# Optimization experiments

Measured on AMD Instinct MI355X. Metric: run time of the kernel, lower is better.

Reference implementation:

```python
import jax, jax.numpy as jnp
import numpy as np

N = 100_000   # nodes
E = 200_000   # directed edges
G = 2_500     # graphs in batch
F_NODE = 16
F_EDGE = 8
H1 = 32
H2 = 16


def setup_inputs() -> dict:
    key = jax.random.key(0)
    ks = jax.random.split(key, 24)
    p = lambda k, shape: 0.1 * jax.random.normal(k, shape, dtype=jnp.float32)
    inp = {
        "x": jax.random.normal(ks[0], (N, F_NODE), dtype=jnp.float32),
        "edge_attr": jax.random.normal(ks[1], (E, F_EDGE), dtype=jnp.float32),
        # edge-MLP for conv1: F_EDGE -> 16 -> F_NODE*H1
        "w_e1a": p(ks[2], (F_EDGE, 16)), "b_e1a": p(ks[3], (16,)),
        "w_e1b": p(ks[4], (16, F_NODE * H1)), "b_e1b": p(ks[5], (F_NODE * H1,)),
        "w_root1": p(ks[6], (F_NODE, H1)), "b_root1": p(ks[7], (H1,)),
        # edge-MLP for conv2: F_EDGE -> 16 -> H1*H2
        "w_e2a": p(ks[8], (F_EDGE, 16)), "b_e2a": p(ks[9], (16,)),
        "w_e2b": p(ks[10], (16, H1 * H2)), "b_e2b": p(ks[11], (H1 * H2,)),
        "w_root2": p(ks[12], (H1, H2)), "b_root2": p(ks[13], (H2,)),
        # attention-pool gate nn: F_NODE -> F_NODE -> 1
        "w_g1": p(ks[14], (F_NODE, F_NODE)), "b_g1": p(ks[15], (F_NODE,)),
        "w_g2": p(ks[16], (F_NODE, 1)), "b_g2": p(ks[17], (1,)),
        # head: (H2 + F_NODE) -> 8 -> 1
        "w_l1": p(ks[18], (H2 + F_NODE, 8)), "b_l1": p(ks[19], (8,)),
        "w_l2": p(ks[20], (8, 1)), "b_l2": p(ks[21], (1,)),
        "edge_index": jax.random.randint(ks[22], (2, E), 0, N),
        "batch": jnp.sort(jax.random.randint(ks[23], (N,), 0, G)),
    }
    return inp


def _nnconv(x, src, tgt, edge_attr, wa, ba, wb, bb, wr, br, in_c, out_c, n):
    # PyG NNConv: x_i' = x_i @ W_root + b + sum_{j->i} x_j @ Theta(e_ji)
    h = jax.nn.relu(edge_attr @ wa + ba)              # [E, 16]
    theta = (h @ wb + bb).reshape(-1, in_c, out_c)    # [E, in, out]
    msg = jnp.einsum('ei,eio->eo', x[src], theta)     # [E, out]
    agg = jax.ops.segment_sum(msg, tgt, num_segments=n)
    return x @ wr + br + agg


def reference(x, edge_attr, w_e1a, b_e1a, w_e1b, b_e1b, w_root1, b_root1,
              w_e2a, b_e2a, w_e2b, b_e2b, w_root2, b_root2,
              w_g1, b_g1, w_g2, b_g2, w_l1, b_l1, w_l2, b_l2,
              edge_index, batch):
    src, tgt = edge_index[0], edge_index[1]
    n = x.shape[0]

    # GlobalAttention pooling on raw node features (per-graph segment softmax)
    gate = jax.nn.relu(x @ w_g1 + b_g1) @ w_g2 + b_g2          # [N, 1]
    m = jax.ops.segment_max(gate, batch, num_segments=G)       # [G, 1]
    a = jnp.exp(gate - m[batch])
    s = jax.ops.segment_sum(a, batch, num_segments=G)
    x_att = jax.ops.segment_sum((a / s[batch]) * x, batch, num_segments=G)  # [G, F_NODE]

    # Two NNConv layers with ReLU
    h = jax.nn.relu(_nnconv(x, src, tgt, edge_attr, w_e1a, b_e1a, w_e1b, b_e1b,
                            w_root1, b_root1, F_NODE, H1, n))
    h = jax.nn.relu(_nnconv(h, src, tgt, edge_attr, w_e2a, b_e2a, w_e2b, b_e2b,
                            w_root2, b_root2, H1, H2, n))

    # global_mean_pool
    cnt = jax.ops.segment_sum(jnp.ones((n, 1), h.dtype), batch, num_segments=G)
    mean = jax.ops.segment_sum(h, batch, num_segments=G) / jnp.maximum(cnt, 1.0)

    z = jnp.concatenate([mean, x_att], axis=1)  # [G, H2 + F_NODE]
    # eval mode: dropout p=0.5 is identity; two linear layers, no activation between
    z = z @ w_l1 + b_l1
    z = z @ w_l2 + b_l2
    return z
```

## Files before the change

### kernel.cpp

```cpp
#include <hip/hip_runtime.h>
#include <hip/hip_bf16.h>

#define NN 100000
#define NE 200000
#define NG 2500
#define FN 16
#define FE 8
#define H1C 32
#define H2C 16
#define KH 16

typedef __attribute__((ext_vector_type(8))) short short8;
typedef __attribute__((ext_vector_type(4))) float f32x4;

__device__ __forceinline__ float bf2f(unsigned int u){
  union { unsigned int i; float f; } v; v.i = (u & 0xffffu) << 16; return v.f;
}
__device__ __forceinline__ unsigned short f2bf(float f){
  union { float f; unsigned int i; } u; u.f = f;
  unsigned int r = u.i + 0x7fffu + ((u.i >> 16) & 1u);
  return (unsigned short)(r >> 16);
}
__device__ __forceinline__ unsigned int pk2(float a, float b){
  return (unsigned int)f2bf(a) | ((unsigned int)f2bf(b) << 16);
}
__device__ __forceinline__ float rdf(const void* p, long i, bool isbf){
  return isbf ? bf2f(((const unsigned short*)p)[i]) : ((const float*)p)[i];
}
__device__ __forceinline__ int lower_bound_i(const int* __restrict__ a, int n, int v){
  int lo = 0, hi = n;
  while(lo < hi){ int mid = (lo + hi) >> 1; if(a[mid] < v) lo = mid + 1; else hi = mid; }
  return lo;
}
__device__ __forceinline__ bool detect_isbf(const void* __restrict__ x){
  const unsigned short* u = (const unsigned short*)x;
  int lane = threadIdx.x & 63;
  float f = bf2f(u[2*lane]);
  float a = fabsf(f);
  bool sane = (f == 0.0f) || (a > 1e-4f && a < 1e4f);
  unsigned long long b = __ballot(sane);
  return __popcll(b) >= 32;
}

#define NW 20
struct WArgs { const void* p[NW]; };
enum {
  OW_E1A=0,     OB_E1A=128,   OW_E1B=144,   OB_E1B=8336,  OW_R1=8848,  OB_R1=9360,
  OW_E2A=9392,  OB_E2A=9520,  OW_E2B=9536,  OB_E2B=17728, OW_R2=18240, OB_R2=18752,
  OW_G1=18768,  OB_G1=19024,  OW_G2=19040,  OB_G2=19056,
  OW_L1=19057,  OB_L1=19313,  OW_L2=19321,  OB_L2=19329
};

#define MB_A 76
#define MB_B (MB_A + 19)
#define MB_C (MB_B + 18)
#define MB_D (MB_C + 391)
#define MB_E (MB_D + 782)
__global__ void __launch_bounds__(256) mega1_kernel(
    const void* __restrict__ xin, const void* __restrict__ efin, WArgs w,
    const int* __restrict__ ei,
    float* __restrict__ wts, unsigned int* __restrict__ wpack1, unsigned int* __restrict__ wpack2,
    float* __restrict__ gate, float* __restrict__ xf, int* __restrict__ deg)
{
  int b = blockIdx.x, tid = threadIdx.x;
  if(b < MB_A){
    bool isbf = detect_isbf(xin);
    int i = b*256 + tid;
    if(i >= 19330) return;
    const int sz[NW] = {128,16,8192,512,512,32, 128,16,8192,512,512,16, 256,16,16,1, 256,8,8,1};
    int seg = 0; long base = 0;
    while(i - base >= sz[seg]){ base += sz[seg]; seg++; }
    wts[i] = rdf(w.p[seg], i - base, isbf);
    return;
  }
  if(b < MB_B){
    bool isbf = detect_isbf(xin);
    int j = (b - MB_A)*256 + tid;
    if(j >= 4736) return;
    int n = j / 148; int k = (j % 148) * 2;
    float v0 = 0.f, v1 = 0.f;
    if(k < 256)        v0 = rdf(w.p[2], (long)k*32 + n, isbf);
    else if(k < 272)   v0 = rdf(w.p[3], (long)(k-256)*32 + n, isbf);
    if(k+1 < 256)      v1 = rdf(w.p[2], (long)(k+1)*32 + n, isbf);
    else if(k+1 < 272) v1 = rdf(w.p[3], (long)(k+1-256)*32 + n, isbf);
    wpack1[j] = pk2(v0, v1);
    return;
  }
  if(b < MB_C){
    bool isbf = detect_isbf(xin);
    int j = (b - MB_B)*256 + tid;
    if(j >= 4416) return;
    int n = j / 276; int k = (j % 276) * 2;
    float v0 = 0.f, v1 = 0.f;
    if(k < 512)        v0 = rdf(w.p[8], (long)k*16 + n, isbf);
    else if(k < 544)   v0 = rdf(w.p[9], (long)(k-512)*16 + n, isbf);
    if(k+1 < 512)      v1 = rdf(w.p[8], (long)(k+1)*16 + n, isbf);
    else if(k+1 < 544) v1 = rdf(w.p[9], (long)(k+1-512)*16 + n, isbf);
    wpack2[j] = pk2(v0, v1);
    return;
  }
  if(b < MB_D){
    __shared__ float s_w1[FN*FN], s_b1[FN], s_w2[FN], s_b2v[1];
    bool isbf = detect_isbf(xin);
    if(tid < FN*FN) s_w1[tid] = rdf(w.p[12], tid, isbf);
    if(tid < FN){ s_b1[tid] = rdf(w.p[13], tid, isbf); s_w2[tid] = rdf(w.p[14], tid, isbf); }
    if(tid == 0) s_b2v[0] = rdf(w.p[15], 0, isbf);
    __syncthreads();
    int n = (b - MB_C)*256 + tid;
    if(n >= NN) return;
    float xv[FN];
    if(isbf){
      uint4 u0 = ((const uint4*)xin)[2*n], u1 = ((const uint4*)xin)[2*n+1];
      xv[0]=bf2f(u0.x); xv[1]=bf2f(u0.x>>16); xv[2]=bf2f(u0.y); xv[3]=bf2f(u0.y>>16);
      xv[4]=bf2f(u0.z); xv[5]=bf2f(u0.z>>16); xv[6]=bf2f(u0.w); xv[7]=bf2f(u0.w>>16);
      xv[8]=bf2f(u1.x); xv[9]=bf2f(u1.x>>16); xv[10]=bf2f(u1.y); xv[11]=bf2f(u1.y>>16);
      xv[12]=bf2f(u1.z); xv[13]=bf2f(u1.z>>16); xv[14]=bf2f(u1.w); xv[15]=bf2f(u1.w>>16);
    } else {
      #pragma unroll
      for(int q = 0; q < 4; q++){
        float4 v = ((const float4*)xin)[4*n + q];
        xv[q*4+0]=v.x; xv[q*4+1]=v.y; xv[q*4+2]=v.z; xv[q*4+3]=v.w;
      }
    }
    float4* xo = (float4*)(xf + (size_t)n*FN);
    #pragma unroll
    for(int q = 0; q < 4; q++) xo[q] = make_float4(xv[q*4+0], xv[q*4+1], xv[q*4+2], xv[q*4+3]);
    float g = s_b2v[0];
    #pragma unroll
    for(int j = 0; j < FN; j++){
      float hj = s_b1[j];
      #pragma unroll
      for(int i = 0; i < FN; i++) hj += xv[i] * s_w1[i*FN + j];
      hj = hj > 0.f ? hj : 0.f;
      g += hj * s_w2[j];
    }
    gate[n] = g;
    return;
  }
  {
    int e = (b - MB_D)*256 + tid;
    if(e < NE) atomicAdd(&deg[ei[NE + e]], 1);
  }
}

#define SCAN_NB 98
__global__ void __launch_bounds__(256) scan_kernel(
    const int* __restrict__ deg, int* __restrict__ rowptr, int* __restrict__ cursor,
    unsigned int* __restrict__ pub)
{
  __shared__ int s_thr[256];
  __shared__ int s_agg[SCAN_NB];
  __shared__ int s_bcast;
  int tid = threadIdx.x, bid = blockIdx.x;
  int base = bid*1024 + tid*4;
  int v0=0, v1=0, v2=0, v3=0;
  if(base + 3 < NN){
    int4 t4 = *(const int4*)(deg + base);
    v0=t4.x; v1=t4.y; v2=t4.z; v3=t4.w;
  } else {
    if(base+0 < NN) v0 = deg[base+0];
    if(base+1 < NN) v1 = deg[base+1];
    if(base+2 < NN) v2 = deg[base+2];
  }
  int e1 = v0, e2 = v0+v1, e3 = v0+v1+v2, tot = v0+v1+v2+v3;
  s_thr[tid] = tot;
  __syncthreads();
  for(int off = 1; off < 256; off <<= 1){
    int t = (tid >= off) ? s_thr[tid-off] : 0;
    __syncthreads();
    s_thr[tid] += t;
    __syncthreads();
  }
  int thr_excl = s_thr[tid] - tot;
  int agg = s_thr[255];
  if(tid == 0) atomicExch(&pub[bid], ((unsigned int)agg << 1) | 1u);
  if(tid < SCAN_NB){
    unsigned int v;
    do { v = atomicAdd(&pub[tid], 0u); } while((v & 1u) == 0u);
    s_agg[tid] = (int)(v >> 1);
  }
  __syncthreads();
  if(tid == 0){
    int acc = 0;
    for(int p = 0; p < bid; p++) acc += s_agg[p];
    s_bcast = acc;
  }
  __syncthreads();
  int ex = s_bcast + thr_excl;
  if(base + 3 < NN){
    int4 r = make_int4(ex, ex+e1, ex+e2, ex+e3);
    *(int4*)(rowptr + base) = r;
    *(int4*)(cursor + base) = r;
  } else {
    if(base+0 < NN){ rowptr[base+0]=ex;    cursor[base+0]=ex;    }
    if(base+1 < NN){ rowptr[base+1]=ex+e1; cursor[base+1]=ex+e1; }
    if(base+2 < NN){ rowptr[base+2]=ex+e2; cursor[base+2]=ex+e2; }
  }
  if(bid == 0 && tid == 0) rowptr[NN] = NE;
}

__global__ void __launch_bounds__(256) fill_edge_kernel(
    const int* __restrict__ ei, int* __restrict__ cursor,
    const void* __restrict__ efin, const float* __restrict__ wts, const void* __restrict__ xin,
    int* __restrict__ srcp, unsigned int* __restrict__ hpk1, unsigned int* __restrict__ hpk2)
{
  __shared__ float s_w1[FE*KH], s_b1[KH], s_w2[FE*KH], s_b2[KH];
  int tid = threadIdx.x;
  if(tid < FE*KH){ s_w1[tid] = wts[OW_E1A + tid]; s_w2[tid] = wts[OW_E2A + tid]; }
  if(tid < KH){ s_b1[tid] = wts[OB_E1A + tid]; s_b2[tid] = wts[OB_E2A + tid]; }
  bool isbf = detect_isbf(xin);
  __syncthreads();
  int e = blockIdx.x*256 + tid;
  if(e >= NE) return;
  int pos = atomicAdd(&cursor[ei[NE + e]], 1);
  srcp[pos] = ei[e];
  float ev[FE];
  if(isbf){
    uint4 u = ((const uint4*)efin)[e];
    ev[0]=bf2f(u.x); ev[1]=bf2f(u.x>>16); ev[2]=bf2f(u.y); ev[3]=bf2f(u.y>>16);
    ev[4]=bf2f(u.z); ev[5]=bf2f(u.z>>16); ev[6]=bf2f(u.w); ev[7]=bf2f(u.w>>16);
  } else {
    float4 a = ((const float4*)efin)[2*e], b = ((const float4*)efin)[2*e+1];
    ev[0]=a.x; ev[1]=a.y; ev[2]=a.z; ev[3]=a.w; ev[4]=b.x; ev[5]=b.y; ev[6]=b.z; ev[7]=b.w;
  }
  unsigned int o[8];
  #pragma unroll
  for(int d = 0; d < 8; d++){
    float h0 = s_b1[2*d], h1 = s_b1[2*d+1];
    #pragma unroll
    for(int k = 0; k < FE; k++){
      h0 += ev[k] * s_w1[k*KH + 2*d];
      h1 += ev[k] * s_w1[k*KH + 2*d+1];
    }
    h0 = h0 > 0.f ? h0 : 0.f; h1 = h1 > 0.f ? h1 : 0.f;
    o[d] = pk2(h0, h1);
  }
  uint4* p1 = (uint4*)(hpk1 + (size_t)pos*8);
  p1[0] = make_uint4(o[0],o[1],o[2],o[3]); p1[1] = make_uint4(o[4],o[5],o[6],o[7]);
  #pragma unroll
  for(int d = 0; d < 8; d++){
    float h0 = s_b2[2*d], h1 = s_b2[2*d+1];
    #pragma unroll
    for(int k = 0; k < FE; k++){
      h0 += ev[k] * s_w2[k*KH + 2*d];
      h1 += ev[k] * s_w2[k*KH + 2*d+1];
    }
    h0 = h0 > 0.f ? h0 : 0.f; h1 = h1 > 0.f ? h1 : 0.f;
    o[d] = pk2(h0, h1);
  }
  uint4* p2 = (uint4*)(hpk2 + (size_t)pos*8);
  p2[0] = make_uint4(o[0],o[1],o[2],o[3]); p2[1] = make_uint4(o[4],o[5],o[6],o[7]);
}

template<int IN, int OUT, bool ABF>
__global__ void __launch_bounds__(256) conv_mfma_kernel(
    const void* __restrict__ nodef, const unsigned int* __restrict__ hpk,
    const int* __restrict__ srcp, const unsigned short* __restrict__ wpack,
    unsigned short* __restrict__ msg)
{
  constexpr int KMF  = ((KH*IN + IN + 31)/32)*32;
  constexpr int KP   = KMF + 8;
  constexpr int NT   = OUT/16;
  constexpr int KS   = KMF/32;
  int tid = threadIdx.x;
  int lane = tid & 63, m = lane & 15, quad = lane >> 4;
  int wid = tid >> 6;
  int ebase = blockIdx.x*64 + wid*16;
  int em = ebase + m;
  int sn = srcp[em];
  int q1 = quad >> 1;
  int xoff = (IN == 16) ? ((quad & 1)*8) : (quad*8);
  float x8[8];
  short8 xb;
  if(ABF){
    uint4 u = *(const uint4*)((const unsigned short*)nodef + (size_t)sn*IN + xoff);
    unsigned int uu[4] = {u.x, u.y, u.z, u.w};
    #pragma unroll
    for(int k = 0; k < 4; k++){ x8[2*k] = bf2f(uu[k]); x8[2*k+1] = bf2f(uu[k] >> 16); }
    xb = *(short8*)&u;
  } else {
    const float4* xp = (const float4*)((const float*)nodef + (size_t)sn*IN + xoff);
    float4 v0 = xp[0], v1 = xp[1];
    x8[0]=v0.x; x8[1]=v0.y; x8[2]=v0.z; x8[3]=v0.w;
    x8[4]=v1.x; x8[5]=v1.y; x8[6]=v1.z; x8[7]=v1.w;
    unsigned int* xbp = (unsigned int*)&xb;
    #pragma unroll
    for(int k = 0; k < 4; k++) xbp[k] = pk2(x8[2*k], x8[2*k+1]);
  }
  unsigned int hu[8];
  {
    const uint4* hp = (const uint4*)(hpk + (size_t)em*8);
    uint4 u0 = hp[0], u1 = hp[1];
    hu[0]=u0.x; hu[1]=u0.y; hu[2]=u0.z; hu[3]=u0.w;
    hu[4]=u1.x; hu[5]=u1.y; hu[6]=u1.z; hu[7]=u1.w;
  }

  f32x4 acc[NT];
  #pragma unroll
  for(int nt = 0; nt < NT; nt++) acc[nt] = (f32x4){0.f,0.f,0.f,0.f};

  #pragma unroll
  for(int ks = 0; ks < KS; ks++){
    short8 a;
    if(ks < KS-1){
      float hv = (IN == 16) ? bf2f(hu[ks] >> (16*q1))
                            : bf2f(hu[ks >> 1] >> (16*(ks & 1)));
      unsigned int* ap = (unsigned int*)&a;
      #pragma unroll
      for(int k = 0; k < 4; k++) ap[k] = pk2(hv*x8[2*k], hv*x8[2*k+1]);
    } else {
      if(IN == 16) a = (quad < 2) ? xb : (short8){0,0,0,0,0,0,0,0};
      else         a = xb;
    }
    #pragma unroll
    for(int nt = 0; nt < NT; nt++){
      short8 b = *(const short8*)(wpack + (size_t)(nt*16 + m)*KP + ks*32 + quad*8);
      acc[nt] = __builtin_amdgcn_mfma_f32_16x16x32_bf16(a, b, acc[nt], 0, 0, 0);
    }
  }
  #pragma unroll
  for(int nt = 0; nt < NT; nt++)
    #pragma unroll
    for(int r = 0; r < 4; r++)
      msg[(size_t)(ebase + quad*4 + r)*OUT + nt*16 + m] = f2bf(acc[nt][r]);
}

__global__ void __launch_bounds__(256) gather1_kernel(
    const float* __restrict__ xf, const unsigned short* __restrict__ msg,
    const int* __restrict__ rowptr,
    const float* __restrict__ wr, const float* __restrict__ br,
    unsigned short* __restrict__ h1b)
{
  __shared__ float s_w[FN*H1C], s_b[H1C];
  for(int i = threadIdx.x; i < FN*H1C; i += 256) s_w[i] = wr[i];
  if(threadIdx.x < H1C) s_b[threadIdx.x] = br[threadIdx.x];
  __syncthreads();
  int g = blockIdx.x*256 + threadIdx.x;
  int n = g >> 3, q = g & 7;
  if(n >= NN) return;
  float a0 = s_b[q*4+0], a1 = s_b[q*4+1], a2 = s_b[q*4+2], a3 = s_b[q*4+3];
  int jb = rowptr[n], je = rowptr[n+1];
  for(int j = jb; j < je; j++){
    const unsigned int* mp = (const unsigned int*)(msg + (size_t)j*H1C + q*4);
    unsigned int u0 = mp[0], u1 = mp[1];
    a0 += bf2f(u0); a1 += bf2f(u0 >> 16); a2 += bf2f(u1); a3 += bf2f(u1 >> 16);
  }
  const float* xr = xf + (size_t)n*FN;
  #pragma unroll
  for(int i = 0; i < FN; i++){
    float xi = xr[i];
    a0 += xi*s_w[i*H1C + q*4+0]; a1 += xi*s_w[i*H1C + q*4+1];
    a2 += xi*s_w[i*H1C + q*4+2]; a3 += xi*s_w[i*H1C + q*4+3];
  }
  a0 = a0>0.f?a0:0.f; a1 = a1>0.f?a1:0.f; a2 = a2>0.f?a2:0.f; a3 = a3>0.f?a3:0.f;
  uint2 hb; hb.x = pk2(a0, a1); hb.y = pk2(a2, a3);
  *(uint2*)(h1b + (size_t)n*H1C + q*4) = hb;
}

__global__ void __launch_bounds__(256) gather2_kernel(
    const unsigned short* __restrict__ h1b, const unsigned short* __restrict__ msg,
    const int* __restrict__ rowptr,
    const float* __restrict__ wr, const float* __restrict__ br, float* __restrict__ h2)
{
  __shared__ float s_w[H1C*H2C], s_b[H2C];
  for(int i = threadIdx.x; i < H1C*H2C; i += 256) s_w[i] = wr[i];
  if(threadIdx.x < H2C) s_b[threadIdx.x] = br[threadIdx.x];
  __syncthreads();
  int g = blockIdx.x*256 + threadIdx.x;
  int n = g >> 2, q = g & 3;
  if(n >= NN) return;
  float a0 = s_b[q*4+0], a1 = s_b[q*4+1], a2 = s_b[q*4+2], a3 = s_b[q*4+3];
  int jb = rowptr[n], je = rowptr[n+1];
  for(int j = jb; j < je; j++){
    const unsigned int* mp = (const unsigned int*)(msg + (size_t)j*H2C + q*4);
    unsigned int u0 = mp[0], u1 = mp[1];
    a0 += bf2f(u0); a1 += bf2f(u0 >> 16); a2 += bf2f(u1); a3 += bf2f(u1 >> 16);
  }
  const unsigned int* hb = (const unsigned int*)(h1b + (size_t)n*H1C);
  #pragma unroll
  for(int i2 = 0; i2 < H1C/2; i2++){
    unsigned int u = hb[i2];
    float x0 = bf2f(u), x1 = bf2f(u >> 16);
    int i = 2*i2;
    a0 += x0*s_w[i*H2C + q*4+0] + x1*s_w[(i+1)*H2C + q*4+0];
    a1 += x0*s_w[i*H2C + q*4+1] + x1*s_w[(i+1)*H2C + q*4+1];
    a2 += x0*s_w[i*H2C + q*4+2] + x1*s_w[(i+1)*H2C + q*4+2];
    a3 += x0*s_w[i*H2C + q*4+3] + x1*s_w[(i+1)*H2C + q*4+3];
  }
  float4 r; r.x = a0>0.f?a0:0.f; r.y = a1>0.f?a1:0.f; r.z = a2>0.f?a2:0.f; r.w = a3>0.f?a3:0.f;
  *(float4*)(h2 + (size_t)n*H2C + q*4) = r;
}

__global__ void head_kernel(const float* __restrict__ gate, const float* __restrict__ xf,
    const float* __restrict__ h2, const int* __restrict__ batch, const void* __restrict__ xin,
    const float* __restrict__ wl1, const float* __restrict__ bl1,
    const float* __restrict__ wl2, const float* __restrict__ bl2,
    void* __restrict__ out)
{
  __shared__ float sz[H2C + FN];
  int g = blockIdx.x;
  int lane = threadIdx.x;
  bool isbf = detect_isbf(xin);
  int start = lower_bound_i(batch, NN, g);
  int end   = lower_bound_i(batch, NN, g + 1);
  float m = -1e30f;
  for(int n = start + lane; n < end; n += 64) m = fmaxf(m, gate[n]);
  #pragma unroll
  for(int o = 32; o >= 1; o >>= 1) m = fmaxf(m, __shfl_xor(m, o));
  float s = 0.f;
  float acc[FN];
  #pragma unroll
  for(int f = 0; f < FN; f++) acc[f] = 0.f;
  for(int n = start + lane; n < end; n += 64){
    float a = __expf(gate[n] - m);
    s += a;
    const float4* xp = (const float4*)(xf + (size_t)n * FN);
    #pragma unroll
    for(int q = 0; q < 4; q++){
      float4 v = xp[q];
      acc[q*4+0] += a*v.x; acc[q*4+1] += a*v.y; acc[q*4+2] += a*v.z; acc[q*4+3] += a*v.w;
    }
  }
  #pragma unroll
  for(int o = 32; o >= 1; o >>= 1){
    s += __shfl_xor(s, o);
    #pragma unroll
    for(int f = 0; f < FN; f++) acc[f] += __shfl_xor(acc[f], o);
  }
  if(lane < FN) sz[H2C + lane] = (end > start && s > 0.f) ? acc[lane] / s : 0.f;
  #pragma unroll
  for(int f = 0; f < H2C; f++) acc[f] = 0.f;
  for(int n = start + lane; n < end; n += 64){
    const float4* hp = (const float4*)(h2 + (size_t)n*H2C);
    #pragma unroll
    for(int q = 0; q < 4; q++){
      float4 v = hp[q];
      acc[q*4+0] += v.x; acc[q*4+1] += v.y; acc[q*4+2] += v.z; acc[q*4+3] += v.w;
    }
  }
  #pragma unroll
  for(int o = 32; o >= 1; o >>= 1){
    #pragma unroll
    for(int f = 0; f < H2C; f++) acc[f] += __shfl_xor(acc[f], o);
  }
  float inv = 1.f / fmaxf((float)(end - start), 1.f);
  if(lane < H2C) sz[lane] = acc[lane] * inv;
  __syncthreads();
  if(lane == 0){
    float t1[8];
    #pragma unroll
    for(int j = 0; j < 8; j++){
      float t = bl1[j];
      #pragma unroll
      for(int c = 0; c < H2C + FN; c++) t += sz[c] * wl1[c*8 + j];
      t1[j] = t;
    }
    float o = bl2[0];
    #pragma unroll
    for(int j = 0; j < 8; j++) o += t1[j] * wl2[j];
    if(isbf) ((__hip_bfloat16*)out)[g] = __float2bfloat16(o);
    else     ((float*)out)[g] = o;
  }
}

extern "C" void kernel_launch(void* const* d_in, const int* in_sizes, int n_in,
                              void* d_out, int out_size, void* d_ws, size_t ws_size,
                              hipStream_t stream)
{
  const int* ei    = (const int*)d_in[22];
  const int* batch = (const int*)d_in[23];

  float* ws = (float*)d_ws;
  float* xf     = ws;
  float* gate   = xf + 1600000;
  float* wts    = gate + 100000;
  int*   rowptr = (int*)(wts + 19360);
  int*   cursor = rowptr + 100016;
  int*   deg    = cursor + 100000;
  unsigned int* pub = (unsigned int*)(deg + 100000);
  int*   srcp   = (int*)(pub + 256);
  unsigned int* wpack1 = (unsigned int*)(srcp + 200000);
  unsigned int* wpack2 = wpack1 + 4736;
  unsigned short* h1b  = (unsigned short*)(wpack2 + 4416);
  unsigned int* hpk1   = (unsigned int*)h1b;
  unsigned short* msg1 = h1b + 3200000;
  unsigned short* msg2 = msg1;
  float* h2     = (float*)(msg1 + 6400000);
  unsigned int* hpk2   = (unsigned int*)h2;

  WArgs wa;
  for(int i = 0; i < NW; i++) wa.p[i] = d_in[2 + i];

  hipMemsetAsync(deg, 0, (100000 + 256)*sizeof(int), stream);
  mega1_kernel<<<MB_E, 256, 0, stream>>>(d_in[0], d_in[1], wa, ei, wts, wpack1, wpack2, gate, xf, deg);
  scan_kernel<<<SCAN_NB, 256, 0, stream>>>(deg, rowptr, cursor, pub);
  fill_edge_kernel<<<(NE + 255)/256, 256, 0, stream>>>(ei, cursor, d_in[1], wts, d_in[0], srcp, hpk1, hpk2);

  conv_mfma_kernel<FN, H1C, false><<<NE/64, 256, 0, stream>>>(
      xf, hpk1, srcp, (const unsigned short*)wpack1, msg1);
  gather1_kernel<<<(NN*8 + 255)/256, 256, 0, stream>>>(xf, msg1, rowptr, wts+OW_R1, wts+OB_R1, h1b);

  conv_mfma_kernel<H1C, H2C, true><<<NE/64, 256, 0, stream>>>(
      h1b, hpk2, srcp, (const unsigned short*)wpack2, msg2);
  gather2_kernel<<<(NN*4 + 255)/256, 256, 0, stream>>>(h1b, msg2, rowptr, wts+OW_R2, wts+OB_R2, h2);

  head_kernel<<<NG, 64, 0, stream>>>(gate, xf, h2, batch, d_in[0],
      wts+OW_L1, wts+OB_L1, wts+OW_L2, wts+OB_L2, d_out);
}
```

Baseline: 211.8 us.

## Switch intermediates to fp16 with packed math and precompute graph start offsets

Replaces bf16 storage and MFMA for edge hidden features, weights, messages and layer-1 activations with fp16. The A operand is now built with packed half multiplies instead of per-element float multiply and bf16 rounding, and conversion uses the hardware cvt_pkrtz instruction. Separately, per-graph start offsets are written in the node pass so the head kernel no longer binary-searches the batch array. fp16 has a narrower range than bf16, so large intermediate values could overflow.

```diff
diff --git a/kernel.cpp b/kernel.cpp
--- a/kernel.cpp
+++ b/kernel.cpp
@@ -12,25 +12,27 @@
 
 typedef __attribute__((ext_vector_type(8))) short short8;
 typedef __attribute__((ext_vector_type(4))) float f32x4;
+typedef _Float16 __attribute__((ext_vector_type(2))) half2v;
+typedef _Float16 __attribute__((ext_vector_type(8))) half8v;
+typedef __fp16 __attribute__((ext_vector_type(2))) pkf16x2;
 
 __device__ __forceinline__ float bf2f(unsigned int u){
   union { unsigned int i; float f; } v; v.i = (u & 0xffffu) << 16; return v.f;
 }
-__device__ __forceinline__ unsigned short f2bf(float f){
-  union { float f; unsigned int i; } u; u.f = f;
-  unsigned int r = u.i + 0x7fffu + ((u.i >> 16) & 1u);
-  return (unsigned short)(r >> 16);
-}
-__device__ __forceinline__ unsigned int pk2(float a, float b){
-  return (unsigned int)f2bf(a) | ((unsigned int)f2bf(b) << 16);
+__device__ __forceinline__ unsigned int pkh(float a, float b){
+  union { pkf16x2 h; unsigned int u; } v; v.h = __builtin_amdgcn_cvt_pkrtz(a, b); return v.u;
+}
+__device__ __forceinline__ unsigned short f2h(float f){
+  union { _Float16 h; unsigned short s; } v; v.h = (_Float16)f; return v.s;
+}
+__device__ __forceinline__ float h2lo(unsigned int u){
+  union { unsigned short s; _Float16 h; } v; v.s = (unsigned short)u; return (float)v.h;
+}
+__device__ __forceinline__ float h2hi(unsigned int u){
+  union { unsigned short s; _Float16 h; } v; v.s = (unsigned short)(u >> 16); return (float)v.h;
 }
 __device__ __forceinline__ float rdf(const void* p, long i, bool isbf){
   return isbf ? bf2f(((const unsigned short*)p)[i]) : ((const float*)p)[i];
-}
-__device__ __forceinline__ int lower_bound_i(const int* __restrict__ a, int n, int v){
-  int lo = 0, hi = n;
-  while(lo < hi){ int mid = (lo + hi) >> 1; if(a[mid] < v) lo = mid + 1; else hi = mid; }
-  return lo;
 }
 __device__ __forceinline__ bool detect_isbf(const void* __restrict__ x){
   const unsigned short* u = (const unsigned short*)x;
@@ -58,9 +60,10 @@
 #define MB_E (MB_D + 782)
 __global__ void __launch_bounds__(256) mega1_kernel(
     const void* __restrict__ xin, const void* __restrict__ efin, WArgs w,
-    const int* __restrict__ ei,
+    const int* __restrict__ ei, const int* __restrict__ batch,
     float* __restrict__ wts, unsigned int* __restrict__ wpack1, unsigned int* __restrict__ wpack2,
-    float* __restrict__ gate, float* __restrict__ xf, int* __restrict__ deg)
+    float* __restrict__ gate, float* __restrict__ xf, int* __restrict__ deg,
+    int* __restrict__ gstart)
 {
   int b = blockIdx.x, tid = threadIdx.x;
   if(b < MB_A){
@@ -83,7 +86,7 @@
     else if(k < 272)   v0 = rdf(w.p[3], (long)(k-256)*32 + n, isbf);
     if(k+1 < 256)      v1 = rdf(w.p[2], (long)(k+1)*32 + n, isbf);
     else if(k+1 < 272) v1 = rdf(w.p[3], (long)(k+1-256)*32 + n, isbf);
-    wpack1[j] = pk2(v0, v1);
+    wpack1[j] = pkh(v0, v1);
     return;
   }
   if(b < MB_C){
@@ -96,7 +99,7 @@
     else if(k < 544)   v0 = rdf(w.p[9], (long)(k-512)*16 + n, isbf);
     if(k+1 < 512)      v1 = rdf(w.p[8], (long)(k+1)*16 + n, isbf);
     else if(k+1 < 544) v1 = rdf(w.p[9], (long)(k+1-512)*16 + n, isbf);
-    wpack2[j] = pk2(v0, v1);
+    wpack2[j] = pkh(v0, v1);
     return;
   }
   if(b < MB_D){
@@ -108,6 +111,12 @@
     __syncthreads();
     int n = (b - MB_C)*256 + tid;
     if(n >= NN) return;
+    {
+      int b1 = batch[n];
+      int b0 = (n == 0) ? -1 : batch[n-1];
+      for(int g2 = b0 + 1; g2 <= b1; g2++) gstart[g2] = n;
+      if(n == NN-1) for(int g2 = b1 + 1; g2 <= NG; g2++) gstart[g2] = NN;
+    }
     float xv[FN];
     if(isbf){
       uint4 u0 = ((const uint4*)xin)[2*n], u1 = ((const uint4*)xin)[2*n+1];
@@ -233,7 +242,7 @@
       h1 += ev[k] * s_w1[k*KH + 2*d+1];
     }
     h0 = h0 > 0.f ? h0 : 0.f; h1 = h1 > 0.f ? h1 : 0.f;
-    o[d] = pk2(h0, h1);
+    o[d] = pkh(h0, h1);
   }
   uint4* p1 = (uint4*)(hpk1 + (size_t)pos*8);
   p1[0] = make_uint4(o[0],o[1],o[2],o[3]); p1[1] = make_uint4(o[4],o[5],o[6],o[7]);
@@ -246,13 +255,13 @@
       h1 += ev[k] * s_w2[k*KH + 2*d+1];
     }
     h0 = h0 > 0.f ? h0 : 0.f; h1 = h1 > 0.f ? h1 : 0.f;
-    o[d] = pk2(h0, h1);
+    o[d] = pkh(h0, h1);
   }
   uint4* p2 = (uint4*)(hpk2 + (size_t)pos*8);
   p2[0] = make_uint4(o[0],o[1],o[2],o[3]); p2[1] = make_uint4(o[4],o[5],o[6],o[7]);
 }
 
-template<int IN, int OUT, bool ABF>
+template<int IN, int OUT, bool AH>
 __global__ void __launch_bounds__(256) conv_mfma_kernel(
     const void* __restrict__ nodef, const unsigned int* __restrict__ hpk,
     const int* __restrict__ srcp, const unsigned short* __restrict__ wpack,
@@ -270,22 +279,17 @@
   int sn = srcp[em];
   int q1 = quad >> 1;
   int xoff = (IN == 16) ? ((quad & 1)*8) : (quad*8);
-  float x8[8];
-  short8 xb;
-  if(ABF){
+  union { half8v v; half2v h[4]; unsigned int w[4]; } X;
+  if(AH){
     uint4 u = *(const uint4*)((const unsigned short*)nodef + (size_t)sn*IN + xoff);
-    unsigned int uu[4] = {u.x, u.y, u.z, u.w};
-    #pragma unroll
-    for(int k = 0; k < 4; k++){ x8[2*k] = bf2f(uu[k]); x8[2*k+1] = bf2f(uu[k] >> 16); }
-    xb = *(short8*)&u;
+    X.w[0]=u.x; X.w[1]=u.y; X.w[2]=u.z; X.w[3]=u.w;
   } else {
     const float4* xp = (const float4*)((const float*)nodef + (size_t)sn*IN + xoff);
     float4 v0 = xp[0], v1 = xp[1];
-    x8[0]=v0.x; x8[1]=v0.y; x8[2]=v0.z; x8[3]=v0.w;
-    x8[4]=v1.x; x8[5]=v1.y; x8[6]=v1.z; x8[7]=v1.w;
-    unsigned int* xbp = (unsigned int*)&xb;
-    #pragma unroll
-    for(int k = 0; k < 4; k++) xbp[k] = pk2(x8[2*k], x8[2*k+1]);
+    X.w[0] = pkh(v0.x, v0.y);
+    X.w[1] = pkh(v0.z, v0.w);
+    X.w[2] = pkh(v1.x, v1.y);
+    X.w[3] = pkh(v1.z, v1.w);
   }
   unsigned int hu[8];
   {
@@ -299,30 +303,32 @@
   #pragma unroll
   for(int nt = 0; nt < NT; nt++) acc[nt] = (f32x4){0.f,0.f,0.f,0.f};
 
+  const half8v hz = {};
   #pragma unroll
   for(int ks = 0; ks < KS; ks++){
-    short8 a;
+    union { half8v v; half2v h[4]; } A;
     if(ks < KS-1){
-      float hv = (IN == 16) ? bf2f(hu[ks] >> (16*q1))
-                            : bf2f(hu[ks >> 1] >> (16*(ks & 1)));
-      unsigned int* ap = (unsigned int*)&a;
+      unsigned short hs = (unsigned short)((IN == 16) ? (hu[ks] >> (16*q1))
+                                                      : (hu[ks >> 1] >> (16*(ks & 1))));
+      union { unsigned short s; _Float16 h; } hc; hc.s = hs;
+      half2v hv2 = { hc.h, hc.h };
       #pragma unroll
-      for(int k = 0; k < 4; k++) ap[k] = pk2(hv*x8[2*k], hv*x8[2*k+1]);
+      for(int k = 0; k < 4; k++) A.h[k] = hv2 * X.h[k];
     } else {
-      if(IN == 16) a = (quad < 2) ? xb : (short8){0,0,0,0,0,0,0,0};
-      else         a = xb;
+      if(IN == 16) A.v = (quad < 2) ? X.v : hz;
+      else         A.v = X.v;
     }
     #pragma unroll
     for(int nt = 0; nt < NT; nt++){
-      short8 b = *(const short8*)(wpack + (size_t)(nt*16 + m)*KP + ks*32 + quad*8);
-      acc[nt] = __builtin_amdgcn_mfma_f32_16x16x32_bf16(a, b, acc[nt], 0, 0, 0);
+      half8v b = *(const half8v*)(wpack + (size_t)(nt*16 + m)*KP + ks*32 + quad*8);
+      acc[nt] = __builtin_amdgcn_mfma_f32_16x16x32_f16(A.v, b, acc[nt], 0, 0, 0);
     }
   }
   #pragma unroll
   for(int nt = 0; nt < NT; nt++)
     #pragma unroll
     for(int r = 0; r < 4; r++)
-      msg[(size_t)(ebase + quad*4 + r)*OUT + nt*16 + m] = f2bf(acc[nt][r]);
+      msg[(size_t)(ebase + quad*4 + r)*OUT + nt*16 + m] = f2h(acc[nt][r]);
 }
 
 __global__ void __launch_bounds__(256) gather1_kernel(
@@ -343,7 +349,7 @@
   for(int j = jb; j < je; j++){
     const unsigned int* mp = (const unsigned int*)(msg + (size_t)j*H1C + q*4);
     unsigned int u0 = mp[0], u1 = mp[1];
-    a0 += bf2f(u0); a1 += bf2f(u0 >> 16); a2 += bf2f(u1); a3 += bf2f(u1 >> 16);
+    a0 += h2lo(u0); a1 += h2hi(u0); a2 += h2lo(u1); a3 += h2hi(u1);
   }
   const float* xr = xf + (size_t)n*FN;
   #pragma unroll
@@ -353,7 +359,7 @@
     a2 += xi*s_w[i*H1C + q*4+2]; a3 += xi*s_w[i*H1C + q*4+3];
   }
   a0 = a0>0.f?a0:0.f; a1 = a1>0.f?a1:0.f; a2 = a2>0.f?a2:0.f; a3 = a3>0.f?a3:0.f;
-  uint2 hb; hb.x = pk2(a0, a1); hb.y = pk2(a2, a3);
+  uint2 hb; hb.x = pkh(a0, a1); hb.y = pkh(a2, a3);
   *(uint2*)(h1b + (size_t)n*H1C + q*4) = hb;
 }
 
@@ -374,13 +380,13 @@
   for(int j = jb; j < je; j++){
     const unsigned int* mp = (const unsigned int*)(msg + (size_t)j*H2C + q*4);
     unsigned int u0 = mp[0], u1 = mp[1];
-    a0 += bf2f(u0); a1 += bf2f(u0 >> 16); a2 += bf2f(u1); a3 += bf2f(u1 >> 16);
+    a0 += h2lo(u0); a1 += h2hi(u0); a2 += h2lo(u1); a3 += h2hi(u1);
   }
   const unsigned int* hb = (const unsigned int*)(h1b + (size_t)n*H1C);
   #pragma unroll
   for(int i2 = 0; i2 < H1C/2; i2++){
     unsigned int u = hb[i2];
-    float x0 = bf2f(u), x1 = bf2f(u >> 16);
+    float x0 = h2lo(u), x1 = h2hi(u);
     int i = 2*i2;
     a0 += x0*s_w[i*H2C + q*4+0] + x1*s_w[(i+1)*H2C + q*4+0];
     a1 += x0*s_w[i*H2C + q*4+1] + x1*s_w[(i+1)*H2C + q*4+1];
@@ -392,7 +398,7 @@
 }
 
 __global__ void head_kernel(const float* __restrict__ gate, const float* __restrict__ xf,
-    const float* __restrict__ h2, const int* __restrict__ batch, const void* __restrict__ xin,
+    const float* __restrict__ h2, const int* __restrict__ gstart, const void* __restrict__ xin,
     const float* __restrict__ wl1, const float* __restrict__ bl1,
     const float* __restrict__ wl2, const float* __restrict__ bl2,
     void* __restrict__ out)
@@ -401,8 +407,8 @@
   int g = blockIdx.x;
   int lane = threadIdx.x;
   bool isbf = detect_isbf(xin);
-  int start = lower_bound_i(batch, NN, g);
-  int end   = lower_bound_i(batch, NN, g + 1);
+  int start = gstart[g];
+  int end   = gstart[g + 1];
   float m = -1e30f;
   for(int n = start + lane; n < end; n += 64) m = fmaxf(m, gate[n]);
   #pragma unroll
@@ -487,12 +493,13 @@
   unsigned short* msg2 = msg1;
   float* h2     = (float*)(msg1 + 6400000);
   unsigned int* hpk2   = (unsigned int*)h2;
+  int*   gstart = (int*)(h2 + 1600000);
 
   WArgs wa;
   for(int i = 0; i < NW; i++) wa.p[i] = d_in[2 + i];
 
   hipMemsetAsync(deg, 0, (100000 + 256)*sizeof(int), stream);
-  mega1_kernel<<<MB_E, 256, 0, stream>>>(d_in[0], d_in[1], wa, ei, wts, wpack1, wpack2, gate, xf, deg);
+  mega1_kernel<<<MB_E, 256, 0, stream>>>(d_in[0], d_in[1], wa, ei, batch, wts, wpack1, wpack2, gate, xf, deg, gstart);
   scan_kernel<<<SCAN_NB, 256, 0, stream>>>(deg, rowptr, cursor, pub);
   fill_edge_kernel<<<(NE + 255)/256, 256, 0, stream>>>(ei, cursor, d_in[1], wts, d_in[0], srcp, hpk1, hpk2);
 
@@ -504,6 +511,6 @@
       h1b, hpk2, srcp, (const unsigned short*)wpack2, msg2);
   gather2_kernel<<<(NN*4 + 255)/256, 256, 0, stream>>>(h1b, msg2, rowptr, wts+OW_R2, wts+OB_R2, h2);
 
-  head_kernel<<<NG, 64, 0, stream>>>(gate, xf, h2, batch, d_in[0],
+  head_kernel<<<NG, 64, 0, stream>>>(gate, xf, h2, gstart, d_in[0],
       wts+OW_L1, wts+OB_L1, wts+OW_L2, wts+OB_L2, d_out);
 }
```

Measured after the change: 212.0 us. No clear change (+0.1%).
